# Optimization experiments

Hardware: AMD Instinct MI355X
Metric: run time of the kernel (lower is better)

Reference implementation:

```python
import jax, jax.numpy as jnp
import numpy as np

B, T, D = 2, 2048, 1024
H = 16
HD = D // H  # 64


def setup_inputs() -> dict:
    key = jax.random.key(0)
    k1, k2, k3, k4, k5 = jax.random.split(key, 5)
    s = 0.02
    return {
        "x": jax.random.normal(k1, (B, T, D), dtype=jnp.float32),
        "Wqkv": jax.random.normal(k2, (D, 3 * D), dtype=jnp.float32) * s,
        "bqkv": jax.random.normal(k3, (3 * D,), dtype=jnp.float32) * s,
        "Wout": jax.random.normal(k4, (D, D), dtype=jnp.float32) * s,
        "bout": jax.random.normal(k5, (D,), dtype=jnp.float32) * s,
    }


def reference(x, Wqkv, bqkv, Wout, bout):
    b, t, c = x.shape
    qkv = (x @ Wqkv + bqkv).reshape(b, t, 3, H, HD)
    q = jnp.transpose(qkv[:, :, 0], (0, 2, 1, 3))  # [B,H,T,HD]
    k = jnp.transpose(qkv[:, :, 1], (0, 2, 1, 3))
    v = jnp.transpose(qkv[:, :, 2], (0, 2, 1, 3))
    att = jnp.einsum("bhqd,bhkd->bhqk", q, k) * (HD ** -0.5)
    mask = jnp.tril(jnp.ones((t, t), dtype=bool))  # causal, no past kv
    att = jnp.where(mask, att, -jnp.inf)
    att = jax.nn.softmax(att, axis=-1)
    y = jnp.einsum("bhqk,bhkd->bhqd", att, v)
    y = jnp.transpose(y, (0, 2, 1, 3)).reshape(b, t, c)
    return y @ Wout + bout
```

## Files before the change

kernel.cpp:

```cpp
#include <hip/hip_runtime.h>
#include <hip/hip_bf16.h>
#include <math.h>

#define B_  2
#define T_  2048
#define D_  1024
#define H_  16
#define HD_ 64

typedef __attribute__((ext_vector_type(8))) short short8;
typedef __attribute__((ext_vector_type(4))) float f32x4;

#if __has_builtin(__builtin_amdgcn_exp2f)
#define EXP2F __builtin_amdgcn_exp2f
#else
#define EXP2F exp2f
#endif

__device__ __forceinline__ ushort f2bf(float x) {
    unsigned u = __builtin_bit_cast(unsigned, x);
    return (ushort)((u + 0x7FFFu + ((u >> 16) & 1u)) >> 16);
}

__device__ __forceinline__ unsigned pack_bf2_fast(float a, float b) {
    unsigned ua = __builtin_bit_cast(unsigned, a) + 0x8000u;
    unsigned ub = __builtin_bit_cast(unsigned, b) + 0x8000u;
    return (ua >> 16) | (ub & 0xFFFF0000u);
}

__device__ __forceinline__ void load_lds_16B(const ushort* g, ushort* l) {
    __builtin_amdgcn_global_load_lds(
        (const __attribute__((address_space(1))) unsigned*)g,
        (__attribute__((address_space(3))) unsigned*)l, 16, 0, 0);
}

__global__ __launch_bounds__(256)
void prep_kernel(const float* __restrict__ x, ushort* __restrict__ xb,
                 const float* __restrict__ Wqkv, ushort* __restrict__ Wqkvt,
                 const float* __restrict__ Wout, ushort* __restrict__ Woutt)
{
    __shared__ ushort Ts[64][65];
    const int bid = blockIdx.x;

    if (bid < 512) {
        const int n4 = (B_ * T_ * D_) / 4;
        for (int i = bid * 256 + threadIdx.x; i < n4; i += 512 * 256) {
            float4 v = ((const float4*)x)[i];
            ushort4 o = { f2bf(v.x), f2bf(v.y), f2bf(v.z), f2bf(v.w) };
            ((ushort4*)xb)[i] = o;
        }
        return;
    }

    const float* W; ushort* Wt; int K, M, m0, k0;
    if (bid < 1280) {
        const int t = bid - 512;
        W = Wqkv; Wt = Wqkvt; K = D_; M = 3 * D_;
        m0 = (t % 48) * 64; k0 = (t / 48) * 64;
    } else {
        const int t = bid - 1280;
        W = Wout; Wt = Woutt; K = D_; M = D_;
        m0 = (t % 16) * 64; k0 = (t / 16) * 64;
    }

    const int tr = threadIdx.x >> 4;
    const int tc = threadIdx.x & 15;
    #pragma unroll
    for (int it = 0; it < 4; it++) {
        int k = tr + it * 16;
        float4 v = *(const float4*)&W[(size_t)(k0 + k) * M + m0 + tc * 4];
        Ts[tc * 4 + 0][k] = f2bf(v.x);
        Ts[tc * 4 + 1][k] = f2bf(v.y);
        Ts[tc * 4 + 2][k] = f2bf(v.z);
        Ts[tc * 4 + 3][k] = f2bf(v.w);
    }
    __syncthreads();
    const int mr = threadIdx.x >> 2;
    const int c4 = threadIdx.x & 3;
    #pragma unroll
    for (int it = 0; it < 4; it++) {
        int kk = c4 * 16 + it * 4;
        ushort4 o = { Ts[mr][kk], Ts[mr][kk + 1], Ts[mr][kk + 2], Ts[mr][kk + 3] };
        *(ushort4*)&Wt[(size_t)(m0 + mr) * K + k0 + kk] = o;
    }
}

template<int MODE>
__global__ __launch_bounds__(256, 4)
void mfma_gemm(const ushort* __restrict__ A, const ushort* __restrict__ Bt,
               const float* __restrict__ bias, float* __restrict__ C,
               ushort* __restrict__ Qg, ushort* __restrict__ Kg,
               ushort* __restrict__ Vtg, int K, int M)
{
    __shared__ __align__(16) ushort lds[8192 + 4096];
    ushort* Asl = lds;
    ushort* Bsl = lds + 8192;

    const int tid = threadIdx.x;
    const int w  = tid >> 6, L = tid & 63;
    const int lt = L & 15, lq = L >> 4;
    const int wr = w >> 1, wc = w & 1;
    const int m0 = blockIdx.x * 64, n0 = blockIdx.y * 128;
    const int rsub = L >> 3;
    const int pgr  = L & 7;

    f32x4 acc[4][2] = {};

    for (int k0 = 0; k0 < K; k0 += 64) {
        __syncthreads();
        #pragma unroll
        for (int j = 0; j < 4; j++) {
            const int row  = (w * 4 + j) * 8 + rsub;
            const int gran = pgr ^ rsub;
            load_lds_16B(A + (size_t)(n0 + row) * K + k0 + gran * 8,
                         &Asl[row * 64 + pgr * 8]);
        }
        #pragma unroll
        for (int j = 0; j < 2; j++) {
            const int row  = (w * 2 + j) * 8 + rsub;
            const int gran = pgr ^ rsub;
            load_lds_16B(Bt + (size_t)(m0 + row) * K + k0 + gran * 8,
                         &Bsl[row * 64 + pgr * 8]);
        }
        __syncthreads();

        #pragma unroll
        for (int ks = 0; ks < 2; ks++) {
            short8 af[4], bf[2];
            #pragma unroll
            for (int i = 0; i < 4; i++) {
                const int ra = wr * 64 + i * 16 + lt;
                af[i] = *(const short8*)&Asl[ra * 64 + (((ks * 4 + lq) ^ (ra & 7)) * 8)];
            }
            #pragma unroll
            for (int j = 0; j < 2; j++) {
                const int rb = wc * 32 + j * 16 + lt;
                bf[j] = *(const short8*)&Bsl[rb * 64 + (((ks * 4 + lq) ^ (rb & 7)) * 8)];
            }
            #pragma unroll
            for (int i = 0; i < 4; i++)
                #pragma unroll
                for (int j = 0; j < 2; j++)
                    acc[i][j] = __builtin_amdgcn_mfma_f32_16x16x32_bf16(af[i], bf[j], acc[i][j], 0, 0, 0);
        }
    }

    if (MODE == 0) {
        #pragma unroll
        for (int j = 0; j < 2; j++) {
            const int m = m0 + wc * 32 + j * 16 + lt;
            const float bv = bias[m];
            #pragma unroll
            for (int i = 0; i < 4; i++) {
                const int n = n0 + wr * 64 + i * 16 + lq * 4;
                #pragma unroll
                for (int r = 0; r < 4; r++)
                    C[(size_t)(n + r) * M + m] = acc[i][j][r] + bv;
            }
        }
    } else {
        const int s = m0 >> 10;
        const float qs = (s == 0) ? 0.18033688011112042f : 1.0f;
        #pragma unroll
        for (int j = 0; j < 2; j++) {
            const int m = m0 + wc * 32 + j * 16 + lt;
            const float bv = bias[m];
            const int h = (m >> 6) & 15, d = m & 63;
            #pragma unroll
            for (int i = 0; i < 4; i++) {
                const int n = n0 + wr * 64 + i * 16 + lq * 4;
                const int b = n >> 11, t = n & 2047;
                if (s < 2) {
                    ushort* dst = (s == 0 ? Qg : Kg);
                    #pragma unroll
                    for (int r = 0; r < 4; r++)
                        dst[((size_t)(b * H_ + h) * T_ + t + r) * HD_ + d] =
                            f2bf((acc[i][j][r] + bv) * qs);
                } else {
                    ushort4 o = { f2bf(acc[i][j][0] + bv), f2bf(acc[i][j][1] + bv),
                                  f2bf(acc[i][j][2] + bv), f2bf(acc[i][j][3] + bv) };
                    *(ushort4*)&Vtg[((size_t)(b * H_ + h) * HD_ + d) * T_ + t] = o;
                }
            }
        }
    }
}

__global__ __launch_bounds__(256, 4)
void attn_mfma(const ushort* __restrict__ Qg, const ushort* __restrict__ Kg,
               const ushort* __restrict__ Vtg, ushort* __restrict__ yb)
{
    const int h = blockIdx.y, b = blockIdx.z;
    const int flip = ((blockIdx.y >> 3) ^ blockIdx.z) & 1;
    const int qb = flip ? blockIdx.x : (31 - blockIdx.x);
    const int tid = threadIdx.x;
    const int w  = tid >> 6, L = tid & 63;
    const int lt = L & 15, lq = L >> 4;
    const int kswz = lt & 7;

    __shared__ __align__(16) ushort Ks [128 * 64];
    __shared__ __align__(16) ushort Vts[64 * 128];
    __shared__ __align__(16) ushort Ps [4][16 * 40];

    const size_t bh = (size_t)(b * H_ + h);
    const ushort* Qbase  = Qg  + bh * T_ * HD_;
    const ushort* Kbase  = Kg  + bh * T_ * HD_;
    const ushort* Vtbase = Vtg + bh * HD_ * T_;

    const int q_glob = qb * 64 + w * 16 + lt;
    const short8 qf0 = *(const short8*)(Qbase + (size_t)q_glob * HD_ + lq * 8);
    const short8 qf1 = *(const short8*)(Qbase + (size_t)q_glob * HD_ + 32 + lq * 8);

    f32x4 acc_o[4] = {};
    float lsum = 0.f;

    const int krow = tid >> 3, kpg = tid & 7;
    const int vrow = tid >> 4, vpg = tid & 15;
    const int nk = (qb + 2) >> 1;

    for (int kb = 0; kb < nk; kb++) {
        __syncthreads();
        #pragma unroll
        for (int rr = 0; rr < 4; rr++) {
            const int row = krow + 32 * rr;
            load_lds_16B(Kbase + (size_t)(kb * 128 + row) * HD_ + (kpg ^ (row & 7)) * 8,
                         &Ks[row * 64 + kpg * 8]);
        }
        #pragma unroll
        for (int rr = 0; rr < 4; rr++) {
            const int d = vrow + 16 * rr;
            load_lds_16B(Vtbase + (size_t)d * T_ + kb * 128 + (vpg ^ (d & 7)) * 8,
                         &Vts[d * 128 + vpg * 8]);
        }
        __syncthreads();

        if (kb < nk - 1) {
            #pragma unroll
            for (int ks = 0; ks < 4; ks++) {
                const int row0 = (2 * ks) * 16 + lt;
                const int row1 = row0 + 16;
                short8 a00 = *(const short8*)&Ks[row0 * 64 + ((lq ^ kswz) * 8)];
                short8 a01 = *(const short8*)&Ks[row0 * 64 + (((4 + lq) ^ kswz) * 8)];
                short8 a10 = *(const short8*)&Ks[row1 * 64 + ((lq ^ kswz) * 8)];
                short8 a11 = *(const short8*)&Ks[row1 * 64 + (((4 + lq) ^ kswz) * 8)];
                f32x4 c0 = {}, c1 = {};
                c0 = __builtin_amdgcn_mfma_f32_16x16x32_bf16(a00, qf0, c0, 0, 0, 0);
                c0 = __builtin_amdgcn_mfma_f32_16x16x32_bf16(a01, qf1, c0, 0, 0, 0);
                c1 = __builtin_amdgcn_mfma_f32_16x16x32_bf16(a10, qf0, c1, 0, 0, 0);
                c1 = __builtin_amdgcn_mfma_f32_16x16x32_bf16(a11, qf1, c1, 0, 0, 0);

                float p0 = EXP2F(c0[0]), p1 = EXP2F(c0[1]);
                float p2 = EXP2F(c0[2]), p3 = EXP2F(c0[3]);
                float p4 = EXP2F(c1[0]), p5 = EXP2F(c1[1]);
                float p6 = EXP2F(c1[2]), p7 = EXP2F(c1[3]);
                lsum += ((p0 + p1) + (p2 + p3)) + ((p4 + p5) + (p6 + p7));
                uint2 pk0 = { pack_bf2_fast(p0, p1), pack_bf2_fast(p2, p3) };
                uint2 pk1 = { pack_bf2_fast(p4, p5), pack_bf2_fast(p6, p7) };
                *(uint2*)&Ps[w][lt * 40 + lq * 4]      = pk0;
                *(uint2*)&Ps[w][lt * 40 + 16 + lq * 4] = pk1;

                short8 pf = *(const short8*)&Ps[w][lt * 40 + lq * 8];

                #pragma unroll
                for (int dt = 0; dt < 4; dt++) {
                    const int vr = dt * 16 + lt;
                    short8 vf = *(const short8*)&Vts[vr * 128 + (((ks * 4 + lq) ^ kswz) * 8)];
                    acc_o[dt] = __builtin_amdgcn_mfma_f32_16x16x32_bf16(pf, vf, acc_o[dt], 0, 0, 0);
                }
            }
        } else {
            const int ksN = (qb & 1) ? 4 : 2;
            const int mk0 = (qb & 1) ? 2 : 0;
            for (int ks = 0; ks < ksN; ks++) {
                const int row0 = (2 * ks) * 16 + lt;
                const int row1 = row0 + 16;
                short8 a00 = *(const short8*)&Ks[row0 * 64 + ((lq ^ kswz) * 8)];
                short8 a01 = *(const short8*)&Ks[row0 * 64 + (((4 + lq) ^ kswz) * 8)];
                short8 a10 = *(const short8*)&Ks[row1 * 64 + ((lq ^ kswz) * 8)];
                short8 a11 = *(const short8*)&Ks[row1 * 64 + (((4 + lq) ^ kswz) * 8)];
                f32x4 c0 = {}, c1 = {};
                c0 = __builtin_amdgcn_mfma_f32_16x16x32_bf16(a00, qf0, c0, 0, 0, 0);
                c0 = __builtin_amdgcn_mfma_f32_16x16x32_bf16(a01, qf1, c0, 0, 0, 0);
                c1 = __builtin_amdgcn_mfma_f32_16x16x32_bf16(a10, qf0, c1, 0, 0, 0);
                c1 = __builtin_amdgcn_mfma_f32_16x16x32_bf16(a11, qf1, c1, 0, 0, 0);

                float p[8];
                #pragma unroll
                for (int r = 0; r < 4; r++) { p[r] = EXP2F(c0[r]); p[4 + r] = EXP2F(c1[r]); }
                if (ks >= mk0) {
                    const int key0 = kb * 128 + (2 * ks) * 16 + lq * 4;
                    #pragma unroll
                    for (int r = 0; r < 4; r++) {
                        if (key0 + r > q_glob)      p[r] = 0.f;
                        if (key0 + 16 + r > q_glob) p[4 + r] = 0.f;
                    }
                }
                lsum += ((p[0] + p[1]) + (p[2] + p[3])) + ((p[4] + p[5]) + (p[6] + p[7]));
                uint2 pk0 = { pack_bf2_fast(p[0], p[1]), pack_bf2_fast(p[2], p[3]) };
                uint2 pk1 = { pack_bf2_fast(p[4], p[5]), pack_bf2_fast(p[6], p[7]) };
                *(uint2*)&Ps[w][lt * 40 + lq * 4]      = pk0;
                *(uint2*)&Ps[w][lt * 40 + 16 + lq * 4] = pk1;

                short8 pf = *(const short8*)&Ps[w][lt * 40 + lq * 8];

                #pragma unroll
                for (int dt = 0; dt < 4; dt++) {
                    const int vr = dt * 16 + lt;
                    short8 vf = *(const short8*)&Vts[vr * 128 + (((ks * 4 + lq) ^ kswz) * 8)];
                    acc_o[dt] = __builtin_amdgcn_mfma_f32_16x16x32_bf16(pf, vf, acc_o[dt], 0, 0, 0);
                }
            }
        }
    }

    lsum += __shfl_xor(lsum, 16, 64);
    lsum += __shfl_xor(lsum, 32, 64);
    const float inv = 1.0f / lsum;

    float linv[4];
    #pragma unroll
    for (int r = 0; r < 4; r++) linv[r] = __shfl(inv, lq * 4 + r, 64);

    ushort* ybase = yb + (size_t)(b * T_ + qb * 64 + w * 16) * D_ + h * HD_;
    #pragma unroll
    for (int r = 0; r < 4; r++)
        #pragma unroll
        for (int dt = 0; dt < 4; dt++)
            ybase[(size_t)(lq * 4 + r) * D_ + dt * 16 + lt] = f2bf(acc_o[dt][r] * linv[r]);
}

extern "C" void kernel_launch(void* const* d_in, const int* in_sizes, int n_in,
                              void* d_out, int out_size, void* d_ws, size_t ws_size,
                              hipStream_t stream)
{
    const float* x    = (const float*)d_in[0];
    const float* Wqkv = (const float*)d_in[1];
    const float* bqkv = (const float*)d_in[2];
    const float* Wout = (const float*)d_in[3];
    const float* bout = (const float*)d_in[4];
    float* out = (float*)d_out;

    char* ws = (char*)d_ws;
    const size_t NT = (size_t)B_ * T_;
    ushort* xb     = (ushort*)ws;
    ushort* Wqkvt  = (ushort*)(ws + NT * D_ * 2);
    ushort* Woutt  = (ushort*)(ws + NT * D_ * 2 + (size_t)3 * D_ * D_ * 2);
    char*   p      = ws + NT * D_ * 2 + (size_t)4 * D_ * D_ * 2;
    const size_t qkv_elems = (size_t)B_ * H_ * T_ * HD_;
    ushort* Qg  = (ushort*)p;
    ushort* Kg  = (ushort*)(p + qkv_elems * 2);
    ushort* Vtg = (ushort*)(p + qkv_elems * 4);
    ushort* yb  = (ushort*)(p + qkv_elems * 6);

    prep_kernel<<<1536, 256, 0, stream>>>(x, xb, Wqkv, Wqkvt, Wout, Woutt);

    mfma_gemm<1><<<dim3(3 * D_ / 64, NT / 128), 256, 0, stream>>>(
        xb, Wqkvt, bqkv, nullptr, Qg, Kg, Vtg, D_, 3 * D_);

    attn_mfma<<<dim3(32, H_, B_), 256, 0, stream>>>(Qg, Kg, Vtg, yb);

    mfma_gemm<0><<<dim3(D_ / 64, NT / 128), 256, 0, stream>>>(
        yb, Woutt, bout, out, nullptr, nullptr, nullptr, D_, D_);
}
```

Baseline: 176.7 us.

## Split QKV and output GEMMs, enlarge QKV tile, stage epilogue stores through LDS

After: 168.9 us. -4.4%, faster.

```diff
diff --git a/kernel.cpp b/kernel.cpp
--- a/kernel.cpp
+++ b/kernel.cpp
@@ -75,23 +75,130 @@
         Ts[tc * 4 + 3][k] = f2bf(v.w);
     }
     __syncthreads();
-    const int mr = threadIdx.x >> 2;
-    const int c4 = threadIdx.x & 3;
     #pragma unroll
-    for (int it = 0; it < 4; it++) {
-        int kk = c4 * 16 + it * 4;
-        ushort4 o = { Ts[mr][kk], Ts[mr][kk + 1], Ts[mr][kk + 2], Ts[mr][kk + 3] };
-        *(ushort4*)&Wt[(size_t)(m0 + mr) * K + k0 + kk] = o;
-    }
-}
-
-template<int MODE>
+    for (int it = 0; it < 2; it++) {
+        const int mr  = (threadIdx.x >> 3) + it * 32;
+        const int seg = (threadIdx.x & 7) * 8;
+        short8 v;
+        #pragma unroll
+        for (int r = 0; r < 8; r++) v[r] = (short)Ts[mr][seg + r];
+        *(short8*)&Wt[(size_t)(m0 + mr) * K + k0 + seg] = v;
+    }
+}
+
 __global__ __launch_bounds__(256, 4)
-void mfma_gemm(const ushort* __restrict__ A, const ushort* __restrict__ Bt,
-               const float* __restrict__ bias, float* __restrict__ C,
-               ushort* __restrict__ Qg, ushort* __restrict__ Kg,
-               ushort* __restrict__ Vtg, int K, int M)
+void gemm_qkv(const ushort* __restrict__ A, const ushort* __restrict__ Bt,
+              const float* __restrict__ bias,
+              ushort* __restrict__ Qg, ushort* __restrict__ Kg,
+              ushort* __restrict__ Vtg)
 {
+    const int K = D_;
+    __shared__ __align__(16) ushort lds[16384];
+    ushort* Asl = lds;
+    ushort* Bsl = lds + 8192;
+
+    const int tid = threadIdx.x;
+    const int w  = tid >> 6, L = tid & 63;
+    const int lt = L & 15, lq = L >> 4;
+    const int wr = w >> 1, wc = w & 1;
+    const int m0 = blockIdx.x * 128, n0 = blockIdx.y * 128;
+    const int rsub = L >> 3;
+    const int pgr  = L & 7;
+
+    f32x4 acc[4][4] = {};
+
+    for (int k0 = 0; k0 < K; k0 += 64) {
+        __syncthreads();
+        #pragma unroll
+        for (int j = 0; j < 4; j++) {
+            const int row  = (w * 4 + j) * 8 + rsub;
+            const int gran = pgr ^ rsub;
+            load_lds_16B(A  + (size_t)(n0 + row) * K + k0 + gran * 8,
+                         &Asl[row * 64 + pgr * 8]);
+            load_lds_16B(Bt + (size_t)(m0 + row) * K + k0 + gran * 8,
+                         &Bsl[row * 64 + pgr * 8]);
+        }
+        __syncthreads();
+
+        #pragma unroll
+        for (int ks = 0; ks < 2; ks++) {
+            short8 af[4], bf[4];
+            #pragma unroll
+            for (int i = 0; i < 4; i++) {
+                const int ra = wr * 64 + i * 16 + lt;
+                af[i] = *(const short8*)&Asl[ra * 64 + (((ks * 4 + lq) ^ (ra & 7)) * 8)];
+                const int rb = wc * 64 + i * 16 + lt;
+                bf[i] = *(const short8*)&Bsl[rb * 64 + (((ks * 4 + lq) ^ (rb & 7)) * 8)];
+            }
+            #pragma unroll
+            for (int i = 0; i < 4; i++)
+                #pragma unroll
+                for (int j = 0; j < 4; j++)
+                    acc[i][j] = __builtin_amdgcn_mfma_f32_16x16x32_bf16(af[i], bf[j], acc[i][j], 0, 0, 0);
+        }
+    }
+
+    __syncthreads();
+    const int s  = m0 >> 10;
+    const int h0 = (m0 & 1023) >> 6;
+    const float qs = (s == 0) ? 0.18033688011112042f : 1.0f;
+
+    if (s < 2) {
+        #pragma unroll
+        for (int j = 0; j < 4; j++) {
+            const int m  = wc * 64 + j * 16 + lt;
+            const float bv = bias[m0 + m];
+            #pragma unroll
+            for (int i = 0; i < 4; i++) {
+                const int n = wr * 64 + i * 16 + lq * 4;
+                #pragma unroll
+                for (int r = 0; r < 4; r++)
+                    lds[(n + r) * 128 + m] = f2bf((acc[i][j][r] + bv) * qs);
+            }
+        }
+        __syncthreads();
+        ushort* dst = (s == 0 ? Qg : Kg);
+        #pragma unroll
+        for (int it = 0; it < 8; it++) {
+            const int g   = tid + it * 256;
+            const int row = g >> 4, c = g & 15;
+            const int n = n0 + row;
+            const int b = n >> 11, t = n & 2047;
+            const int h = h0 + (c >> 3), d = (c & 7) * 8;
+            short8 v = *(const short8*)&lds[row * 128 + c * 8];
+            *(short8*)&dst[((size_t)(b * H_ + h) * T_ + t) * HD_ + d] = v;
+        }
+    } else {
+        #pragma unroll
+        for (int j = 0; j < 4; j++) {
+            const int m  = wc * 64 + j * 16 + lt;
+            const float bv = bias[m0 + m];
+            #pragma unroll
+            for (int i = 0; i < 4; i++) {
+                const int n = wr * 64 + i * 16 + lq * 4;
+                uint2 pk = { pack_bf2_fast(acc[i][j][0] + bv, acc[i][j][1] + bv),
+                             pack_bf2_fast(acc[i][j][2] + bv, acc[i][j][3] + bv) };
+                *(uint2*)&lds[m * 128 + n] = pk;
+            }
+        }
+        __syncthreads();
+        const int b = n0 >> 11, t0 = n0 & 2047;
+        #pragma unroll
+        for (int it = 0; it < 8; it++) {
+            const int g   = tid + it * 256;
+            const int row = g >> 4, c = g & 15;
+            const int h = h0 + (row >> 6), d = row & 63;
+            short8 v = *(const short8*)&lds[row * 128 + c * 8];
+            *(short8*)&Vtg[((size_t)(b * H_ + h) * HD_ + d) * T_ + t0 + c * 8] = v;
+        }
+    }
+}
+
+__global__ __launch_bounds__(256, 4)
+void gemm_out(const ushort* __restrict__ A, const ushort* __restrict__ Bt,
+              const float* __restrict__ bias, float* __restrict__ C)
+{
+    const int K = D_, M = D_;
     __shared__ __align__(16) ushort lds[8192 + 4096];
     ushort* Asl = lds;
     ushort* Bsl = lds + 8192;
@@ -104,7 +211,7 @@
     const int rsub = L >> 3;
     const int pgr  = L & 7;
 
-    f32x4 acc[4][2] = {};
+    f32x4 acc[2][4] = {};
 
     for (int k0 = 0; k0 < K; k0 += 64) {
         __syncthreads();
@@ -126,62 +233,35 @@
 
         #pragma unroll
         for (int ks = 0; ks < 2; ks++) {
-            short8 af[4], bf[2];
+            short8 wf[2], yf[4];
+            #pragma unroll
+            for (int j = 0; j < 2; j++) {
+                const int rb = wc * 32 + j * 16 + lt;
+                wf[j] = *(const short8*)&Bsl[rb * 64 + (((ks * 4 + lq) ^ (rb & 7)) * 8)];
+            }
             #pragma unroll
             for (int i = 0; i < 4; i++) {
                 const int ra = wr * 64 + i * 16 + lt;
-                af[i] = *(const short8*)&Asl[ra * 64 + (((ks * 4 + lq) ^ (ra & 7)) * 8)];
-            }
-            #pragma unroll
-            for (int j = 0; j < 2; j++) {
-                const int rb = wc * 32 + j * 16 + lt;
-                bf[j] = *(const short8*)&Bsl[rb * 64 + (((ks * 4 + lq) ^ (rb & 7)) * 8)];
-            }
-            #pragma unroll
-            for (int i = 0; i < 4; i++)
-                #pragma unroll
-                for (int j = 0; j < 2; j++)
-                    acc[i][j] = __builtin_amdgcn_mfma_f32_16x16x32_bf16(af[i], bf[j], acc[i][j], 0, 0, 0);
-        }
-    }
-
-    if (MODE == 0) {
-        #pragma unroll
-        for (int j = 0; j < 2; j++) {
-            const int m = m0 + wc * 32 + j * 16 + lt;
-            const float bv = bias[m];
-            #pragma unroll
-            for (int i = 0; i < 4; i++) {
-                const int n = n0 + wr * 64 + i * 16 + lq * 4;
-                #pragma unroll
-                for (int r = 0; r < 4; r++)
-                    C[(size_t)(n + r) * M + m] = acc[i][j][r] + bv;
-            }
-        }
-    } else {
-        const int s = m0 >> 10;
-        const float qs = (s == 0) ? 0.18033688011112042f : 1.0f;
-        #pragma unroll
-        for (int j = 0; j < 2; j++) {
-            const int m = m0 + wc * 32 + j * 16 + lt;
-            const float bv = bias[m];
-            const int h = (m >> 6) & 15, d = m & 63;
-            #pragma unroll
-            for (int i = 0; i < 4; i++) {
-                const int n = n0 + wr * 64 + i * 16 + lq * 4;
-                const int b = n >> 11, t = n & 2047;
-                if (s < 2) {
-                    ushort* dst = (s == 0 ? Qg : Kg);
-                    #pragma unroll
-                    for (int r = 0; r < 4; r++)
-                        dst[((size_t)(b * H_ + h) * T_ + t + r) * HD_ + d] =
-                            f2bf((acc[i][j][r] + bv) * qs);
-                } else {
-                    ushort4 o = { f2bf(acc[i][j][0] + bv), f2bf(acc[i][j][1] + bv),
-                                  f2bf(acc[i][j][2] + bv), f2bf(acc[i][j][3] + bv) };
-                    *(ushort4*)&Vtg[((size_t)(b * H_ + h) * HD_ + d) * T_ + t] = o;
-                }
-            }
+                yf[i] = *(const short8*)&Asl[ra * 64 + (((ks * 4 + lq) ^ (ra & 7)) * 8)];
+            }
+            #pragma unroll
+            for (int j = 0; j < 2; j++)
+                #pragma unroll
+                for (int i = 0; i < 4; i++)
+                    acc[j][i] = __builtin_amdgcn_mfma_f32_16x16x32_bf16(wf[j], yf[i], acc[j][i], 0, 0, 0);
+        }
+    }
+
+    #pragma unroll
+    for (int j = 0; j < 2; j++) {
+        const int mbase = m0 + wc * 32 + j * 16 + lq * 4;
+        const float4 bv = *(const float4*)&bias[mbase];
+        #pragma unroll
+        for (int i = 0; i < 4; i++) {
+            const int n = n0 + wr * 64 + i * 16 + lt;
+            float4 o = { acc[j][i][0] + bv.x, acc[j][i][1] + bv.y,
+                         acc[j][i][2] + bv.z, acc[j][i][3] + bv.w };
+            *(float4*)&C[(size_t)n * M + mbase] = o;
         }
     }
 }
@@ -354,11 +434,11 @@
 
     prep_kernel<<<1536, 256, 0, stream>>>(x, xb, Wqkv, Wqkvt, Wout, Woutt);
 
-    mfma_gemm<1><<<dim3(3 * D_ / 64, NT / 128), 256, 0, stream>>>(
-        xb, Wqkvt, bqkv, nullptr, Qg, Kg, Vtg, D_, 3 * D_);
+    gemm_qkv<<<dim3(3 * D_ / 128, NT / 128), 256, 0, stream>>>(
+        xb, Wqkvt, bqkv, Qg, Kg, Vtg);
 
     attn_mfma<<<dim3(32, H_, B_), 256, 0, stream>>>(Qg, Kg, Vtg, yb);
 
-    mfma_gemm<0><<<dim3(D_ / 64, NT / 128), 256, 0, stream>>>(
-        yb, Woutt, bout, out, nullptr, nullptr, nullptr, D_, D_);
-}
+    gemm_out<<<dim3(D_ / 64, NT / 128), 256, 0, stream>>>(
+        yb, Woutt, bout, out);
+}
```
